# Optimization experiments

Measured on AMD Instinct MI355X. Metric: run time of the kernel, lower is better.

## Reference

```python
import jax, jax.numpy as jnp
import numpy as np

B, N, C = 16, 1024, 256
NH, DH = 8, 32          # dense attention heads
NHD, P = 8, 4           # deformable heads / sampling points
Hs = Ws = 32            # value spatial grid (N == Hs*Ws)
HID = 1024              # mlp hidden = 4*C


def setup_inputs() -> dict:
    key = jax.random.key(0)
    ks = jax.random.split(key, 16)
    rn = lambda i, shape, s=1.0: jax.random.normal(ks[i], shape, jnp.float32) * s
    return {
        "x": rn(0, (B, N, C)),
        "ref": jax.random.uniform(ks[1], (B, N, 2), jnp.float32),
        "value": rn(2, (B, N, C)),
        "ln1_w": jnp.ones((C,), jnp.float32), "ln1_b": jnp.zeros((C,), jnp.float32),
        "ln2_w": jnp.ones((C,), jnp.float32), "ln2_b": jnp.zeros((C,), jnp.float32),
        "ln3_w": jnp.ones((C,), jnp.float32), "ln3_b": jnp.zeros((C,), jnp.float32),
        "qkv_w": rn(3, (3 * C, C), 0.05),
        "proj_w": rn(4, (C, C), 0.05), "proj_b": jnp.zeros((C,), jnp.float32),
        "off_w": rn(5, (NHD * P * 2, C), 0.01), "off_b": rn(6, (NHD * P * 2,), 0.5),
        "aw_w": rn(7, (NHD * P, C), 0.01), "aw_b": jnp.zeros((NHD * P,), jnp.float32),
        "vproj_w": rn(8, (C, C), 0.05), "vproj_b": jnp.zeros((C,), jnp.float32),
        "oproj_w": rn(9, (C, C), 0.05), "oproj_b": jnp.zeros((C,), jnp.float32),
        "fc1_w": rn(10, (HID, C), 0.05), "fc1_b": jnp.zeros((HID,), jnp.float32),
        "fc2_w": rn(11, (C, HID), 0.05), "fc2_b": jnp.zeros((C,), jnp.float32),
    }


def _ln(x, w, b):
    m = x.mean(-1, keepdims=True)
    v = ((x - m) ** 2).mean(-1, keepdims=True)
    return (x - m) * jax.lax.rsqrt(v + 1e-5) * w + b


def _attn(x, qkv_w, proj_w, proj_b):
    qkv = (x @ qkv_w.T).reshape(B, N, 3, NH, DH)
    q, k, v = qkv[:, :, 0], qkv[:, :, 1], qkv[:, :, 2]
    a = jnp.einsum('bqhd,bkhd->bhqk', q, k) * (DH ** -0.5)
    a = jax.nn.softmax(a, axis=-1)
    o = jnp.einsum('bhqk,bkhd->bqhd', a, v).reshape(B, N, C)
    return o @ proj_w.T + proj_b


def _deform(q, ref, value, off_w, off_b, aw_w, aw_b, vproj_w, vproj_b, oproj_w, oproj_b):
    # single-level MS deformable attention (Deformable-DETR style)
    v = (value @ vproj_w.T + vproj_b).reshape(B, Hs * Ws, NHD, DH)
    off = (q @ off_w.T + off_b).reshape(B, N, NHD, P, 2)
    aw = jax.nn.softmax((q @ aw_w.T + aw_b).reshape(B, N, NHD, P), axis=-1)
    norm = jnp.array([Ws, Hs], jnp.float32)
    loc = ref[:, :, None, None, :] + off / norm  # [B,N,NHD,P,2] normalized coords
    gx = loc[..., 0] * Ws - 0.5
    gy = loc[..., 1] * Hs - 0.5
    x0 = jnp.floor(gx); y0 = jnp.floor(gy)
    lx = gx - x0; ly = gy - y0
    x0i = x0.astype(jnp.int32); y0i = y0.astype(jnp.int32)
    b_idx = jnp.arange(B)[:, None, None, None]
    h_idx = jnp.arange(NHD)[None, None, :, None]

    def gather(xi, yi):
        valid = ((xi >= 0) & (xi < Ws) & (yi >= 0) & (yi < Hs)).astype(jnp.float32)
        idx = jnp.clip(yi, 0, Hs - 1) * Ws + jnp.clip(xi, 0, Ws - 1)
        return v[b_idx, idx, h_idx] * valid[..., None]  # [B,N,NHD,P,DH]

    s = (gather(x0i, y0i) * ((1 - lx) * (1 - ly))[..., None]
         + gather(x0i + 1, y0i) * (lx * (1 - ly))[..., None]
         + gather(x0i, y0i + 1) * ((1 - lx) * ly)[..., None]
         + gather(x0i + 1, y0i + 1) * (lx * ly)[..., None])
    out = (s * aw[..., None]).sum(axis=3).reshape(B, N, C)
    return out @ oproj_w.T + oproj_b


def reference(x, ref, value, ln1_w, ln1_b, ln2_w, ln2_b, ln3_w, ln3_b,
              qkv_w, proj_w, proj_b, off_w, off_b, aw_w, aw_b,
              vproj_w, vproj_b, oproj_w, oproj_b, fc1_w, fc1_b, fc2_w, fc2_b):
    x = x + _attn(_ln(x, ln1_w, ln1_b), qkv_w, proj_w, proj_b)
    x = x + _deform(_ln(x, ln2_w, ln2_b), ref, value,
                    off_w, off_b, aw_w, aw_b, vproj_w, vproj_b, oproj_w, oproj_b)
    h = jax.nn.gelu(_ln(x, ln3_w, ln3_b) @ fc1_w.T + fc1_b, approximate=False) @ fc2_w.T + fc2_b
    return x + h
```

## Files before the change

### kernel.cpp

```cpp
#include <hip/hip_runtime.h>
#include <hip/hip_bf16.h>

#define Bq   16
#define Nq   1024
#define Cq   256
#define NHq  8
#define DHq  32
#define HIDq 1024
#define BNq  (Bq * Nq)

typedef float f32x4 __attribute__((ext_vector_type(4)));
typedef short bf16x8 __attribute__((ext_vector_type(8)));
typedef unsigned short ushort_t;

__device__ __forceinline__ unsigned int f2bf(float f) {
    unsigned int u = __builtin_bit_cast(unsigned int, f);
    u = (u + 0x7fffu + ((u >> 16) & 1u)) >> 16;
    return u & 0xffffu;
}
__device__ __forceinline__ unsigned int packbf2(float a, float b) {
    unsigned int ua = __builtin_bit_cast(unsigned int, a) + 0x8000u;
    unsigned int ub = __builtin_bit_cast(unsigned int, b) + 0x8000u;
    return __builtin_amdgcn_perm(ub, ua, 0x07060302);
}
__device__ __forceinline__ float gelu_t(float x) {
    float y = x * (0.7978845608028654f + 0.035677408136300125f * x * x);
    float e = __builtin_amdgcn_exp2f(y * 2.8853900817779268f);
    return x - x / (1.f + e);
}

typedef __attribute__((address_space(1))) const unsigned int* gas_u32;
typedef __attribute__((address_space(3))) unsigned int* las_u32;
__device__ __forceinline__ void gload16(const void* g, void* l) {
    __builtin_amdgcn_global_load_lds((gas_u32)g, (las_u32)l, 16, 0, 0);
}

struct CastSeg { const float* src; ushort_t* dst; int nblk; int n; };
struct CastArgs { CastSeg s[9]; };

__global__ __launch_bounds__(256) void castm(CastArgs a) {
    int bid = blockIdx.x;
    int seg = 0, acc = 0;
    for (seg = 0; seg < 9; seg++) {
        if (bid < acc + a.s[seg].nblk) break;
        acc += a.s[seg].nblk;
    }
    const CastSeg sg = a.s[seg];
    int i = (bid - acc) * 1024 + threadIdx.x * 4;
    if (i < sg.n) {
        float4 v = *(const float4*)(sg.src + i);
        uint2 u;
        u.x = packbf2(v.x, v.y);
        u.y = packbf2(v.z, v.w);
        *(uint2*)(sg.dst + i) = u;
    }
}

__global__ __launch_bounds__(256) void ln_kernel(const float* __restrict__ X,
                                                 const float* __restrict__ w,
                                                 const float* __restrict__ b,
                                                 ushort_t* __restrict__ Y) {
    int wave = threadIdx.x >> 6, lane = threadIdx.x & 63;
    int t = blockIdx.x * 4 + wave;
    float4 v = *(const float4*)(X + (size_t)t * Cq + lane * 4);
    float s = v.x + v.y + v.z + v.w;
#pragma unroll
    for (int d = 1; d < 64; d <<= 1) s += __shfl_xor(s, d);
    float mean = s * (1.f / 256.f);
    float4 dv = {v.x - mean, v.y - mean, v.z - mean, v.w - mean};
    float q = dv.x * dv.x + dv.y * dv.y + dv.z * dv.z + dv.w * dv.w;
#pragma unroll
    for (int d = 1; d < 64; d <<= 1) q += __shfl_xor(q, d);
    float rs = rsqrtf(q * (1.f / 256.f) + 1e-5f);
    float4 wv = *(const float4*)(w + lane * 4);
    float4 bv = *(const float4*)(b + lane * 4);
    uint2 u;
    u.x = packbf2(dv.x * rs * wv.x + bv.x, dv.y * rs * wv.y + bv.y);
    u.y = packbf2(dv.z * rs * wv.z + bv.z, dv.w * rs * wv.w + bv.w);
    *(uint2*)(Y + (size_t)t * Cq + lane * 4) = u;
}

template <int OMODE, bool GELU_, bool RESID, int KT>
__global__ __launch_bounds__(256) void mgemm(const ushort_t* __restrict__ A,
                                             const ushort_t* __restrict__ W,
                                             const float* __restrict__ bias,
                                             const float* __restrict__ R,
                                             void* __restrict__ OutP,
                                             int M, int Nn) {
    __shared__ __align__(16) ushort_t Al[4096];
    __shared__ __align__(16) ushort_t Bl[4096];
    int m0 = blockIdx.x * 128, n0 = blockIdx.y * 128;
    int tid = threadIdx.x;
    int w = tid >> 6, lane = tid & 63;
    int l15 = lane & 15, quad = lane >> 4;
    int wrow = w >> 1, wcol = w & 1;

    f32x4 acc[4][4];
#pragma unroll
    for (int i = 0; i < 4; i++)
#pragma unroll
        for (int j = 0; j < 4; j++) acc[i][j] = (f32x4){0.f, 0.f, 0.f, 0.f};

    const ushort_t* gA0 = A + (size_t)(m0 + lane) * KT + w * 8;
    const ushort_t* gA1 = A + (size_t)(m0 + 64 + lane) * KT + w * 8;
    const ushort_t* gB0 = W + (size_t)(n0 + lane) * KT + w * 8;
    const ushort_t* gB1 = W + (size_t)(n0 + 64 + lane) * KT + w * 8;
    ushort_t* lA0 = &Al[(w * 128) * 8];
    ushort_t* lA1 = &Al[(w * 128 + 64) * 8];
    ushort_t* lB0 = &Bl[(w * 128) * 8];
    ushort_t* lB1 = &Bl[(w * 128 + 64) * 8];

#pragma unroll
    for (int k0 = 0; k0 < KT; k0 += 32) {
        gload16(gA0 + k0, lA0);
        gload16(gA1 + k0, lA1);
        gload16(gB0 + k0, lB0);
        gload16(gB1 + k0, lB1);
        __syncthreads();

        bf16x8 aF[4], bF[4];
#pragma unroll
        for (int i = 0; i < 4; i++)
            aF[i] = *(const bf16x8*)&Al[(quad * 128 + wrow * 64 + i * 16 + l15) * 8];
#pragma unroll
        for (int j = 0; j < 4; j++)
            bF[j] = *(const bf16x8*)&Bl[(quad * 128 + wcol * 64 + j * 16 + l15) * 8];
#pragma unroll
        for (int i = 0; i < 4; i++)
#pragma unroll
            for (int j = 0; j < 4; j++)
                acc[i][j] = __builtin_amdgcn_mfma_f32_16x16x32_bf16(bF[j], aF[i], acc[i][j], 0, 0, 0);
        __syncthreads();
    }

#pragma unroll
    for (int i = 0; i < 4; i++) {
        int mg = m0 + wrow * 64 + i * 16 + l15;
#pragma unroll
        for (int j = 0; j < 4; j++) {
            int ng = n0 + wcol * 64 + j * 16 + quad * 4;
            if (ng >= Nn) continue;
            f32x4 rv = acc[i][j];
            if constexpr (OMODE == 1) {
                int which = ng >> 8;
                int h = (ng >> 5) & 7;
                int d = ng & 31;
                int bb = mg >> 10, nn = mg & 1023;
                ushort_t* qb = (ushort_t*)OutP;
                if (which == 2) {
                    size_t dst = 2 * (size_t)BNq * Cq +
                                 ((size_t)(bb * 8 + h) * 32 + d) * 1024 + nn;
#pragma unroll
                    for (int r = 0; r < 4; r++)
                        qb[dst + (size_t)r * 1024] = (ushort_t)f2bf(rv[r]);
                } else {
                    if (which == 0) {
                        const float sc = 0.17677669529663687f * 1.4426950408889634f;
                        rv[0] *= sc; rv[1] *= sc; rv[2] *= sc; rv[3] *= sc;
                    }
                    size_t dst = (size_t)which * ((size_t)BNq * Cq) +
                                 ((size_t)(bb * 8 + h) * 1024 + nn) * 32 + d;
                    uint2 pk;
                    pk.x = packbf2(rv[0], rv[1]);
                    pk.y = packbf2(rv[2], rv[3]);
                    *(uint2*)(qb + dst) = pk;
                }
            } else {
                if (bias) {
                    float4 bv = *(const float4*)(bias + ng);
                    rv[0] += bv.x; rv[1] += bv.y; rv[2] += bv.z; rv[3] += bv.w;
                }
                if (GELU_) {
#pragma unroll
                    for (int r = 0; r < 4; r++) rv[r] = gelu_t(rv[r]);
                }
                if constexpr (OMODE == 2) {
                    uint2 pk;
                    pk.x = packbf2(rv[0], rv[1]);
                    pk.y = packbf2(rv[2], rv[3]);
                    *(uint2*)((ushort_t*)OutP + (size_t)mg * Nn + ng) = pk;
                } else {
                    if (RESID) {
                        float4 rr = *(const float4*)(R + (size_t)mg * Nn + ng);
                        rv[0] += rr.x; rv[1] += rr.y; rv[2] += rr.z; rv[3] += rr.w;
                    }
                    *(float4*)((float*)OutP + (size_t)mg * Nn + ng) =
                        make_float4(rv[0], rv[1], rv[2], rv[3]);
                }
            }
        }
    }
}

__global__ __launch_bounds__(256) void attn_mfma(const ushort_t* __restrict__ Qb,
                                                 const ushort_t* __restrict__ Kb,
                                                 const ushort_t* __restrict__ Vtg,
                                                 ushort_t* __restrict__ o) {
    int bh = blockIdx.x;
    int b = bh >> 3, h = bh & 7;
    int q0 = blockIdx.y * 128;
    int tid = threadIdx.x;
    int wave = tid >> 6, lane = tid & 63;
    int l15 = lane & 15, quad = lane >> 4;

    __shared__ __align__(16) ushort_t Ks[64][40];
    __shared__ __align__(16) ushort_t Vs[32][88];
    __shared__ __align__(16) ushort_t Ps[4][32][72];

    const size_t hb = (size_t)bh * 32768;

    bf16x8 qfrag[2];
#pragma unroll
    for (int g = 0; g < 2; g++)
        qfrag[g] = *(const bf16x8*)(Qb + hb + (size_t)(q0 + wave * 32 + g * 16 + l15) * 32 + quad * 8);

    f32x4 oa[2][2];
#pragma unroll
    for (int g = 0; g < 2; g++)
#pragma unroll
        for (int t = 0; t < 2; t++) oa[g][t] = (f32x4){0.f, 0.f, 0.f, 0.f};
    float lsum[2] = {0.f, 0.f};

    int krow = tid >> 2, kch = tid & 3;
    int vrow = tid >> 3, vch = tid & 7;
    const ushort_t* kgp = Kb + hb + (size_t)krow * 32 + kch * 8;
    const ushort_t* vgp = Vtg + hb + (size_t)vrow * 1024 + vch * 8;

    for (int kt = 0; kt < 16; kt++) {
        __syncthreads();
        *(bf16x8*)&Ks[krow][kch * 8] = *(const bf16x8*)(kgp + kt * 64 * 32);
        *(bf16x8*)&Vs[vrow][vch * 8] = *(const bf16x8*)(vgp + kt * 64);
        __syncthreads();

        bf16x8 kf[4];
#pragma unroll
        for (int kg = 0; kg < 4; kg++)
            kf[kg] = *(const bf16x8*)&Ks[kg * 16 + l15][quad * 8];

        f32x4 z = {0.f, 0.f, 0.f, 0.f};
#pragma unroll
        for (int g = 0; g < 2; g++) {
#pragma unroll
            for (int kg = 0; kg < 4; kg++) {
                f32x4 st = __builtin_amdgcn_mfma_f32_16x16x32_bf16(kf[kg], qfrag[g], z, 0, 0, 0);
                float e0 = __builtin_amdgcn_exp2f(st[0]);
                float e1 = __builtin_amdgcn_exp2f(st[1]);
                float e2 = __builtin_amdgcn_exp2f(st[2]);
                float e3 = __builtin_amdgcn_exp2f(st[3]);
                lsum[g] += (e0 + e1) + (e2 + e3);
                uint2 pk;
                pk.x = packbf2(e0, e1);
                pk.y = packbf2(e2, e3);
                *(uint2*)&Ps[wave][g * 16 + l15][kg * 16 + quad * 4] = pk;
            }
        }
#pragma unroll
        for (int c = 0; c < 2; c++) {
            bf16x8 vb0 = *(const bf16x8*)&Vs[l15][c * 32 + quad * 8];
            bf16x8 vb1 = *(const bf16x8*)&Vs[16 + l15][c * 32 + quad * 8];
#pragma unroll
            for (int g = 0; g < 2; g++) {
                bf16x8 pa = *(const bf16x8*)&Ps[wave][g * 16 + l15][c * 32 + quad * 8];
                oa[g][0] = __builtin_amdgcn_mfma_f32_16x16x32_bf16(pa, vb0, oa[g][0], 0, 0, 0);
                oa[g][1] = __builtin_amdgcn_mfma_f32_16x16x32_bf16(pa, vb1, oa[g][1], 0, 0, 0);
            }
        }
    }

#pragma unroll
    for (int g = 0; g < 2; g++) {
        float rs = lsum[g];
        rs += __shfl_xor(rs, 16);
        rs += __shfl_xor(rs, 32);
        lsum[g] = rs;
    }
#pragma unroll
    for (int g = 0; g < 2; g++) {
#pragma unroll
        for (int r = 0; r < 4; r++) {
            float inv = 1.f / __shfl(lsum[g], quad * 4 + r);
            int q = q0 + wave * 32 + g * 16 + quad * 4 + r;
            ushort_t* orow = o + ((size_t)(b * 1024 + q)) * 256 + h * 32;
            orow[l15] = (ushort_t)f2bf(oa[g][0][r] * inv);
            orow[l15 + 16] = (ushort_t)f2bf(oa[g][1][r] * inv);
        }
    }
}

__global__ __launch_bounds__(256) void deform_kernel(const float* __restrict__ ref,
                                                     const float* __restrict__ off,
                                                     const float* __restrict__ awl,
                                                     const float* __restrict__ v,
                                                     ushort_t* __restrict__ out) {
    int t = blockIdx.x;
    int b = t >> 10;
    int tid = threadIdx.x;
    int h = tid >> 5, d = tid & 31;

    float rx = ref[(size_t)t * 2 + 0];
    float ry = ref[(size_t)t * 2 + 1];
    const float* offr = off + (size_t)t * 64 + h * 8;
    const float* awr = awl + (size_t)t * 32 + h * 4;

    float L0 = awr[0], L1 = awr[1], L2 = awr[2], L3 = awr[3];
    float mm = fmaxf(fmaxf(L0, L1), fmaxf(L2, L3));
    float e0 = __expf(L0 - mm), e1 = __expf(L1 - mm), e2 = __expf(L2 - mm), e3 = __expf(L3 - mm);
    float inv = 1.f / (e0 + e1 + e2 + e3);
    float aw[4] = {e0 * inv, e1 * inv, e2 * inv, e3 * inv};

    const float* vb = v + (size_t)b * Nq * Cq + h * 32 + d;

    float s = 0.f;
#pragma unroll
    for (int p = 0; p < 4; p++) {
        float gx = rx * 32.f + offr[p * 2 + 0] - 0.5f;
        float gy = ry * 32.f + offr[p * 2 + 1] - 0.5f;
        float x0f = floorf(gx), y0f = floorf(gy);
        float lx = gx - x0f, ly = gy - y0f;
        int x0 = (int)x0f, y0 = (int)y0f;
        auto g = [&](int xi, int yi) -> float {
            if (xi < 0 || xi > 31 || yi < 0 || yi > 31) return 0.f;
            return vb[(size_t)(yi * 32 + xi) * Cq];
        };
        float sp = g(x0, y0) * (1.f - lx) * (1.f - ly)
                 + g(x0 + 1, y0) * lx * (1.f - ly)
                 + g(x0, y0 + 1) * (1.f - lx) * ly
                 + g(x0 + 1, y0 + 1) * lx * ly;
        s += aw[p] * sp;
    }
    out[(size_t)t * Cq + h * 32 + d] = (ushort_t)f2bf(s);
}

extern "C" void kernel_launch(void* const* d_in, const int* in_sizes, int n_in,
                              void* d_out, int out_size, void* d_ws, size_t ws_size,
                              hipStream_t stream) {
    const size_t S = (size_t)BNq * Cq;
    float* ws = (float*)d_ws;
    float* X = ws;
    ushort_t* Ybf = (ushort_t*)(ws + S);
    ushort_t* Wbf = (ushort_t*)(ws + S + S / 2);

    ushort_t* Wqkv   = Wbf;
    ushort_t* Wproj  = Wbf + 196608;
    ushort_t* Woff   = Wbf + 262144;
    ushort_t* Waw    = Wbf + 278528;
    ushort_t* Wvproj = Wbf + 286720;
    ushort_t* Woproj = Wbf + 352256;
    ushort_t* Wfc1   = Wbf + 417792;
    ushort_t* Wfc2   = Wbf + 679936;

    ushort_t* QKVbf = (ushort_t*)(ws + 2 * S);
    ushort_t* O1bf  = (ushort_t*)(ws + 2 * S + 3 * S / 2);
    float* Vb   = ws + 2 * S + S / 2;
    float* OffB = ws + 2 * S + 3 * S / 2;
    float* AwB  = OffB + (size_t)BNq * 64;
    ushort_t* Sbbf = (ushort_t*)(AwB + (size_t)BNq * 32);
    ushort_t* Hbbf = (ushort_t*)(ws + 2 * S);
    ushort_t* Valbf = (ushort_t*)(ws + 9 * S / 2);

    auto fp = [&](int i) { return (const float*)d_in[i]; };
    const float* x_in = fp(0);

    CastArgs ca;
    ca.s[0] = {fp(9),  Wqkv,   192, 196608};
    ca.s[1] = {fp(10), Wproj,  64,  65536};
    ca.s[2] = {fp(12), Woff,   16,  16384};
    ca.s[3] = {fp(14), Waw,    8,   8192};
    ca.s[4] = {fp(16), Wvproj, 64,  65536};
    ca.s[5] = {fp(18), Woproj, 64,  65536};
    ca.s[6] = {fp(20), Wfc1,   256, 262144};
    ca.s[7] = {fp(22), Wfc2,   256, 262144};
    ca.s[8] = {fp(2),  Valbf,  4096, (int)S};
    castm<<<5016, 256, 0, stream>>>(ca);

    ln_kernel<<<BNq / 4, 256, 0, stream>>>(x_in, fp(3), fp(4), Ybf);
    mgemm<1, false, false, 256><<<dim3(128, 6), 256, 0, stream>>>(
        Ybf, Wqkv, nullptr, nullptr, QKVbf, BNq, 768);
    attn_mfma<<<dim3(128, 8), 256, 0, stream>>>(
        QKVbf, QKVbf + S, QKVbf + 2 * S, O1bf);
    mgemm<0, false, true, 256><<<dim3(128, 2), 256, 0, stream>>>(
        O1bf, Wproj, fp(11), x_in, X, BNq, 256);

    ln_kernel<<<BNq / 4, 256, 0, stream>>>(X, fp(5), fp(6), Ybf);
    mgemm<0, false, false, 256><<<dim3(128, 2), 256, 0, stream>>>(
        Valbf, Wvproj, fp(17), nullptr, Vb, BNq, 256);
    mgemm<0, false, false, 256><<<dim3(128, 1), 256, 0, stream>>>(
        Ybf, Woff, fp(13), nullptr, OffB, BNq, 64);
    mgemm<0, false, false, 256><<<dim3(128, 1), 256, 0, stream>>>(
        Ybf, Waw, fp(15), nullptr, AwB, BNq, 32);
    deform_kernel<<<BNq, 256, 0, stream>>>(fp(1), OffB, AwB, Vb, Sbbf);
    mgemm<0, false, true, 256><<<dim3(128, 2), 256, 0, stream>>>(
        Sbbf, Woproj, fp(19), X, X, BNq, 256);

    ln_kernel<<<BNq / 4, 256, 0, stream>>>(X, fp(7), fp(8), Ybf);
    mgemm<2, true, false, 256><<<dim3(128, 8), 256, 0, stream>>>(
        Ybf, Wfc1, fp(21), nullptr, Hbbf, BNq, 1024);
    mgemm<0, false, true, 1024><<<dim3(128, 2), 256, 0, stream>>>(
        Hbbf, Wfc2, fp(23), X, d_out, BNq, 256);
}
```

Measured before the change: 361.6 us.

## Load K/V fragments directly from global and compute softmax row sums via MFMA

Drops the shared-memory staging of K and V tiles in the dense attention kernel, along with its two block barriers per tile. Each wave now loads its K and V MFMA fragments straight from global memory and register-prefetches the next K tile. The softmax denominator is no longer a scalar exp sum with shuffles: it is an extra MFMA of the bf16 probability tile against a ones vector, so it matches the rounded weights actually used. The cost is redundant global/L2 reads across the four waves and extra register pressure.

```diff
diff --git a/kernel.cpp b/kernel.cpp
--- a/kernel.cpp
+++ b/kernel.cpp
@@ -203,8 +203,6 @@
     int wave = tid >> 6, lane = tid & 63;
     int l15 = lane & 15, quad = lane >> 4;
 
-    __shared__ __align__(16) ushort_t Ks[64][40];
-    __shared__ __align__(16) ushort_t Vs[32][88];
     __shared__ __align__(16) ushort_t Ps[4][32][72];
 
     const size_t hb = (size_t)bh * 32768;
@@ -214,30 +212,34 @@
     for (int g = 0; g < 2; g++)
         qfrag[g] = *(const bf16x8*)(Qb + hb + (size_t)(q0 + wave * 32 + g * 16 + l15) * 32 + quad * 8);
 
+    const ushort_t* kfp = Kb + hb + (size_t)l15 * 32 + quad * 8;
+    const ushort_t* vfp0 = Vtg + hb + (size_t)l15 * 1024 + quad * 8;
+    const ushort_t* vfp1 = Vtg + hb + (size_t)(l15 + 16) * 1024 + quad * 8;
+
+    bf16x8 ones;
+#pragma unroll
+    for (int i = 0; i < 8; i++) ones[i] = (short)0x3F80;
+
     f32x4 oa[2][2];
 #pragma unroll
     for (int g = 0; g < 2; g++)
 #pragma unroll
         for (int t = 0; t < 2; t++) oa[g][t] = (f32x4){0.f, 0.f, 0.f, 0.f};
-    float lsum[2] = {0.f, 0.f};
-
-    int krow = tid >> 2, kch = tid & 3;
-    int vrow = tid >> 3, vch = tid & 7;
-    const ushort_t* kgp = Kb + hb + (size_t)krow * 32 + kch * 8;
-    const ushort_t* vgp = Vtg + hb + (size_t)vrow * 1024 + vch * 8;
+    f32x4 osum[2] = {(f32x4){0.f, 0.f, 0.f, 0.f}, (f32x4){0.f, 0.f, 0.f, 0.f}};
+
+    bf16x8 kf[4];
+#pragma unroll
+    for (int kg = 0; kg < 4; kg++)
+        kf[kg] = *(const bf16x8*)(kfp + (size_t)(kg * 16) * 32);
 
     for (int kt = 0; kt < 16; kt++) {
-        __syncthreads();
-        *(bf16x8*)&Ks[krow][kch * 8] = *(const bf16x8*)(kgp + kt * 64 * 32);
-        *(bf16x8*)&Vs[vrow][vch * 8] = *(const bf16x8*)(vgp + kt * 64);
-        __syncthreads();
-
-        bf16x8 kf[4];
-#pragma unroll
-        for (int kg = 0; kg < 4; kg++)
-            kf[kg] = *(const bf16x8*)&Ks[kg * 16 + l15][quad * 8];
-
-        f32x4 z = {0.f, 0.f, 0.f, 0.f};
+        bf16x8 kfn[4];
+        if (kt < 15) {
+#pragma unroll
+            for (int kg = 0; kg < 4; kg++)
+                kfn[kg] = *(const bf16x8*)(kfp + (size_t)((kt + 1) * 64 + kg * 16) * 32);
+        }
+        const f32x4 z = {0.f, 0.f, 0.f, 0.f};
 #pragma unroll
         for (int g = 0; g < 2; g++) {
 #pragma unroll
@@ -247,7 +249,6 @@
                 float e1 = __builtin_amdgcn_exp2f(st[1]);
                 float e2 = __builtin_amdgcn_exp2f(st[2]);
                 float e3 = __builtin_amdgcn_exp2f(st[3]);
-                lsum[g] += (e0 + e1) + (e2 + e3);
                 uint2 pk;
                 pk.x = packbf2(e0, e1);
                 pk.y = packbf2(e2, e3);
@@ -256,29 +257,25 @@
         }
 #pragma unroll
         for (int c = 0; c < 2; c++) {
-            bf16x8 vb0 = *(const bf16x8*)&Vs[l15][c * 32 + quad * 8];
-            bf16x8 vb1 = *(const bf16x8*)&Vs[16 + l15][c * 32 + quad * 8];
+            bf16x8 vb0 = *(const bf16x8*)(vfp0 + kt * 64 + c * 32);
+            bf16x8 vb1 = *(const bf16x8*)(vfp1 + kt * 64 + c * 32);
 #pragma unroll
             for (int g = 0; g < 2; g++) {
                 bf16x8 pa = *(const bf16x8*)&Ps[wave][g * 16 + l15][c * 32 + quad * 8];
                 oa[g][0] = __builtin_amdgcn_mfma_f32_16x16x32_bf16(pa, vb0, oa[g][0], 0, 0, 0);
                 oa[g][1] = __builtin_amdgcn_mfma_f32_16x16x32_bf16(pa, vb1, oa[g][1], 0, 0, 0);
+                osum[g] = __builtin_amdgcn_mfma_f32_16x16x32_bf16(pa, ones, osum[g], 0, 0, 0);
             }
         }
+#pragma unroll
+        for (int kg = 0; kg < 4; kg++) kf[kg] = kfn[kg];
     }
 
 #pragma unroll
     for (int g = 0; g < 2; g++) {
-        float rs = lsum[g];
-        rs += __shfl_xor(rs, 16);
-        rs += __shfl_xor(rs, 32);
-        lsum[g] = rs;
-    }
-#pragma unroll
-    for (int g = 0; g < 2; g++) {
 #pragma unroll
         for (int r = 0; r < 4; r++) {
-            float inv = 1.f / __shfl(lsum[g], quad * 4 + r);
+            float inv = 1.f / osum[g][r];
             int q = q0 + wave * 32 + g * 16 + quad * 4 + r;
             ushort_t* orow = o + ((size_t)(b * 1024 + q)) * 256 + h * 32;
             orow[l15] = (ushort_t)f2bf(oa[g][0][r] * inv);
```

Measured after the change: 375.1 us. 1.04x slower.

## Fuse offset and attention-weight GEMMs and double the GEMM k-step per barrier

Applied to the files above, without the earlier changes.

The generic MFMA GEMM now stages 64 k-elements per shared-memory fill instead of 32. That halves the number of barrier pairs per tile, at the cost of twice the LDS per block. A new output mode computes the sampling-offset and attention-weight projections in one launch over 96 output columns, adding each part's own bias and writing both results. This relies on the two weight matrices and the two output buffers being laid out contiguously. The generic bounds check on output columns is removed, which assumes every other GEMM uses a column count that is a multiple of 128.

```diff
diff --git a/kernel.cpp b/kernel.cpp
--- a/kernel.cpp
+++ b/kernel.cpp
@@ -87,8 +87,8 @@
                                              const float* __restrict__ R,
                                              void* __restrict__ OutP,
                                              int M, int Nn) {
-    __shared__ __align__(16) ushort_t Al[4096];
-    __shared__ __align__(16) ushort_t Bl[4096];
+    __shared__ __align__(16) ushort_t Al[8192];
+    __shared__ __align__(16) ushort_t Bl[8192];
     int m0 = blockIdx.x * 128, n0 = blockIdx.y * 128;
     int tid = threadIdx.x;
     int w = tid >> 6, lane = tid & 63;
@@ -105,31 +105,42 @@
     const ushort_t* gA1 = A + (size_t)(m0 + 64 + lane) * KT + w * 8;
     const ushort_t* gB0 = W + (size_t)(n0 + lane) * KT + w * 8;
     const ushort_t* gB1 = W + (size_t)(n0 + 64 + lane) * KT + w * 8;
-    ushort_t* lA0 = &Al[(w * 128) * 8];
-    ushort_t* lA1 = &Al[(w * 128 + 64) * 8];
-    ushort_t* lB0 = &Bl[(w * 128) * 8];
-    ushort_t* lB1 = &Bl[(w * 128 + 64) * 8];
-
-#pragma unroll
-    for (int k0 = 0; k0 < KT; k0 += 32) {
+    ushort_t* lA0  = &Al[(w * 128) * 8];
+    ushort_t* lA1  = &Al[(w * 128 + 64) * 8];
+    ushort_t* lA0h = &Al[((w + 4) * 128) * 8];
+    ushort_t* lA1h = &Al[((w + 4) * 128 + 64) * 8];
+    ushort_t* lB0  = &Bl[(w * 128) * 8];
+    ushort_t* lB1  = &Bl[(w * 128 + 64) * 8];
+    ushort_t* lB0h = &Bl[((w + 4) * 128) * 8];
+    ushort_t* lB1h = &Bl[((w + 4) * 128 + 64) * 8];
+
+#pragma unroll
+    for (int k0 = 0; k0 < KT; k0 += 64) {
         gload16(gA0 + k0, lA0);
         gload16(gA1 + k0, lA1);
+        gload16(gA0 + k0 + 32, lA0h);
+        gload16(gA1 + k0 + 32, lA1h);
         gload16(gB0 + k0, lB0);
         gload16(gB1 + k0, lB1);
+        gload16(gB0 + k0 + 32, lB0h);
+        gload16(gB1 + k0 + 32, lB1h);
         __syncthreads();
 
-        bf16x8 aF[4], bF[4];
-#pragma unroll
-        for (int i = 0; i < 4; i++)
-            aF[i] = *(const bf16x8*)&Al[(quad * 128 + wrow * 64 + i * 16 + l15) * 8];
-#pragma unroll
-        for (int j = 0; j < 4; j++)
-            bF[j] = *(const bf16x8*)&Bl[(quad * 128 + wcol * 64 + j * 16 + l15) * 8];
-#pragma unroll
-        for (int i = 0; i < 4; i++)
+#pragma unroll
+        for (int ks = 0; ks < 2; ks++) {
+            bf16x8 aF[4], bF[4];
+#pragma unroll
+            for (int i = 0; i < 4; i++)
+                aF[i] = *(const bf16x8*)&Al[((ks * 4 + quad) * 128 + wrow * 64 + i * 16 + l15) * 8];
 #pragma unroll
             for (int j = 0; j < 4; j++)
-                acc[i][j] = __builtin_amdgcn_mfma_f32_16x16x32_bf16(bF[j], aF[i], acc[i][j], 0, 0, 0);
+                bF[j] = *(const bf16x8*)&Bl[((ks * 4 + quad) * 128 + wcol * 64 + j * 16 + l15) * 8];
+#pragma unroll
+            for (int i = 0; i < 4; i++)
+#pragma unroll
+                for (int j = 0; j < 4; j++)
+                    acc[i][j] = __builtin_amdgcn_mfma_f32_16x16x32_bf16(bF[j], aF[i], acc[i][j], 0, 0, 0);
+        }
         __syncthreads();
     }
 
@@ -139,7 +150,6 @@
 #pragma unroll
         for (int j = 0; j < 4; j++) {
             int ng = n0 + wcol * 64 + j * 16 + quad * 4;
-            if (ng >= Nn) continue;
             f32x4 rv = acc[i][j];
             if constexpr (OMODE == 1) {
                 int which = ng >> 8;
@@ -164,6 +174,19 @@
                     pk.x = packbf2(rv[0], rv[1]);
                     pk.y = packbf2(rv[2], rv[3]);
                     *(uint2*)(qb + dst) = pk;
+                }
+            } else if constexpr (OMODE == 3) {
+                if (ng >= 96) continue;
+                if (ng < 64) {
+                    float4 bv = *(const float4*)(bias + ng);
+                    rv[0] += bv.x; rv[1] += bv.y; rv[2] += bv.z; rv[3] += bv.w;
+                    *(float4*)((float*)OutP + (size_t)mg * 64 + ng) =
+                        make_float4(rv[0], rv[1], rv[2], rv[3]);
+                } else {
+                    float4 bv = *(const float4*)(R + (ng - 64));
+                    rv[0] += bv.x; rv[1] += bv.y; rv[2] += bv.z; rv[3] += bv.w;
+                    *(float4*)((float*)OutP + (size_t)BNq * 64 + (size_t)mg * 32 + (ng - 64)) =
+                        make_float4(rv[0], rv[1], rv[2], rv[3]);
                 }
             } else {
                 if (bias) {
@@ -237,7 +260,7 @@
         for (int kg = 0; kg < 4; kg++)
             kf[kg] = *(const bf16x8*)&Ks[kg * 16 + l15][quad * 8];
 
-        f32x4 z = {0.f, 0.f, 0.f, 0.f};
+        const f32x4 z = {0.f, 0.f, 0.f, 0.f};
 #pragma unroll
         for (int g = 0; g < 2; g++) {
 #pragma unroll
@@ -384,10 +407,8 @@
     ln_kernel<<<BNq / 4, 256, 0, stream>>>(X, fp(5), fp(6), Ybf);
     mgemm<0, false, false, 256><<<dim3(128, 2), 256, 0, stream>>>(
         Valbf, Wvproj, fp(17), nullptr, Vb, BNq, 256);
-    mgemm<0, false, false, 256><<<dim3(128, 1), 256, 0, stream>>>(
-        Ybf, Woff, fp(13), nullptr, OffB, BNq, 64);
-    mgemm<0, false, false, 256><<<dim3(128, 1), 256, 0, stream>>>(
-        Ybf, Waw, fp(15), nullptr, AwB, BNq, 32);
+    mgemm<3, false, false, 256><<<dim3(128, 1), 256, 0, stream>>>(
+        Ybf, Woff, fp(13), fp(15), OffB, BNq, 96);
     deform_kernel<<<BNq, 256, 0, stream>>>(fp(1), OffB, AwB, Vb, Sbbf);
     mgemm<0, false, true, 256><<<dim3(128, 2), 256, 0, stream>>>(
         Sbbf, Woproj, fp(19), X, X, BNq, 256);
```

After: 342.6 us. -5.3%, faster.
